# Performance work log

Measured on AMD Instinct MI355X. Metric: run time of the kernel, lower is better.

The kernel has to match this reference:

```python
import jax, jax.numpy as jnp
import numpy as np

N_QUERY = 100000
N_VALUE = 100000
N_DIM = 128
B, LQ, LK = 256, 50, 200
SIGMA = 1.0      # lognormal scale hyperparameter
LN_EPS = 1e-5    # torch LayerNorm default eps


def setup_inputs() -> dict:
    key = jax.random.key(0)
    ks = jax.random.split(key, 7)
    return {
        "Q_idx": jax.random.randint(ks[0], (B, LQ), 0, N_QUERY),
        "K_idx": jax.random.randint(ks[1], (B, LK), 0, N_VALUE),
        "V_idx": jax.random.randint(ks[2], (B, LK), 0, N_VALUE),
        "W_q": jax.random.normal(ks[3], (N_QUERY, N_DIM), dtype=jnp.float32) * 0.02,
        "W_k": jax.random.normal(ks[4], (N_VALUE, N_DIM), dtype=jnp.float32) * 0.02,
        "W_v": jax.random.normal(ks[5], (N_VALUE, N_DIM), dtype=jnp.float32) * 0.02,
        "ln_gamma": jnp.ones((N_DIM,), dtype=jnp.float32),
        "ln_beta": jnp.zeros((N_DIM,), dtype=jnp.float32),
        "eps_noise": jax.random.normal(ks[6], (B, LQ, LK), dtype=jnp.float32),
    }


def reference(Q_idx, K_idx, V_idx, W_q, W_k, W_v, ln_gamma, ln_beta, eps_noise):
    d = W_q.shape[-1]
    q = W_q[Q_idx]                                   # [B, Lq, d]
    k = W_k[K_idx]                                   # [B, Lk, d]
    logits = jnp.einsum("bqd,bkd->bqk", q, k) / jnp.sqrt(jnp.asarray(d, q.dtype))
    log_phi = jax.nn.log_softmax(logits, axis=-1)    # [B, Lq, Lk]
    # reparameterized LogNormal sample with mean phi: exp(log phi - sigma^2/2 + sigma*eps)
    score = jnp.exp(log_phi - 0.5 * SIGMA * SIGMA + SIGMA * eps_noise)
    weight = score / jnp.sum(score, axis=-1, keepdims=True)
    v = W_v[V_idx]                                   # [B, Lk, d]
    context = jnp.einsum("bqk,bkd->bqd", weight, v)  # [B, Lq, d]
    mu = jnp.mean(context, axis=-1, keepdims=True)
    var = jnp.mean(jnp.square(context - mu), axis=-1, keepdims=True)
    normed = (context - mu) * jax.lax.rsqrt(var + LN_EPS)
    return normed * ln_gamma + ln_beta
```

## Files before the change

### kernel.cpp

```cpp
#include <hip/hip_runtime.h>
#include <hip/hip_bf16.h>
#include <cstdint>

namespace {
constexpr int NB    = 256;
constexpr int LQ    = 50;
constexpr int LK    = 200;
constexpr int DIM   = 128;
constexpr int NWAVE = 8;
constexpr int NTHR  = NWAVE * 64;
constexpr int LSTR  = 204;
constexpr int KSTR  = 136;
constexpr int NKR   = 208;
constexpr int NQR   = 64;
constexpr int VG    = 8;
constexpr int NG    = LK / VG;
constexpr int KPW   = LK / NWAVE;
}

typedef __attribute__((ext_vector_type(8))) short bf16x8;
typedef __attribute__((ext_vector_type(4))) float f32x4;

__device__ __forceinline__ float bflo(uint32_t u) { return __uint_as_float(u << 16); }
__device__ __forceinline__ float bfhi(uint32_t u) { return __uint_as_float(u & 0xFFFF0000u); }
__device__ __forceinline__ uint32_t f2bf(float f) {
    uint32_t x = __float_as_uint(f);
    return (x + 0x7FFFu + ((x >> 16) & 1u)) >> 16;
}

__device__ __forceinline__ void run_f32(
    const int* __restrict__ Qi, const int* __restrict__ Ki, const int* __restrict__ Vi,
    const void* __restrict__ Wq, const void* __restrict__ Wk, const void* __restrict__ Wv,
    const void* __restrict__ gm, const void* __restrict__ bt, const void* __restrict__ ep,
    void* __restrict__ out, float* __restrict__ lds,
    uint16_t* __restrict__ ksh, uint16_t* __restrict__ qsh, int* __restrict__ vix)
{
    const int b    = blockIdx.x;
    const int tid  = threadIdx.x;
    const int w    = tid >> 6;
    const int lane = tid & 63;

    for (int i = tid; i < LK; i += NTHR) vix[i] = Vi[b * LK + i];

    #pragma unroll
    for (int j = 0; j < NKR / NWAVE; ++j) {
        const int r = w + NWAVE * j;
        uint32_t v = 0u;
        if (r < LK) {
            const int kidx = Ki[b * LK + r];
            const float2 f = ((const float2*)((const float*)Wk + (size_t)kidx * DIM))[lane];
            v = f2bf(f.x) | (f2bf(f.y) << 16);
        }
        *(uint32_t*)(ksh + (size_t)r * KSTR + 2 * lane) = v;
    }
    #pragma unroll
    for (int j = 0; j < NQR / NWAVE; ++j) {
        const int r = w + NWAVE * j;
        uint32_t v = 0u;
        if (r < LQ) {
            const int qidx = Qi[b * LQ + r];
            const float2 f = ((const float2*)((const float*)Wq + (size_t)qidx * DIM))[lane];
            v = f2bf(f.x) | (f2bf(f.y) << 16);
        }
        *(uint32_t*)(qsh + (size_t)r * KSTR + 2 * lane) = v;
    }
    __syncthreads();

    {
        const int m   = w >> 1;
        const int l15 = lane & 15;
        const int g   = lane >> 4;

        const uint16_t* qbase = qsh + (size_t)(m * 16 + l15) * KSTR + g * 8;
        bf16x8 afr[4];
        #pragma unroll
        for (int ks = 0; ks < 4; ++ks)
            afr[ks] = *(const bf16x8*)(qbase + ks * 32);

        #pragma unroll 1
        for (int n = (w & 1); n < 13; n += 2) {
            const uint16_t* kbase = ksh + (size_t)(n * 16 + l15) * KSTR + g * 8;
            f32x4 acc = {0.f, 0.f, 0.f, 0.f};
            #pragma unroll
            for (int ks = 0; ks < 4; ++ks) {
                const bf16x8 bfr = *(const bf16x8*)(kbase + ks * 32);
                acc = __builtin_amdgcn_mfma_f32_16x16x32_bf16(afr[ks], bfr, acc, 0, 0, 0);
            }
            const int kcol = n * 16 + l15;
            #pragma unroll
            for (int r = 0; r < 4; ++r) {
                const int q = m * 16 + g * 4 + r;
                if (q < LQ && kcol < LK)
                    lds[q * LSTR + kcol] = acc[r] * 0.08838834764831843f;
            }
        }
    }
    __syncthreads();

    for (int q = w; q < LQ; q += NWAVE) {
        float z[4];
        float m = -INFINITY;
        #pragma unroll
        for (int i = 0; i < 4; ++i) {
            const int k = i * 64 + lane;
            if (k < LK) {
                const float e = ((const float*)ep)[(size_t)(b * LQ + q) * LK + k];
                z[i] = lds[q * LSTR + k] + e;
                m = fmaxf(m, z[i]);
            } else z[i] = -INFINITY;
        }
        #pragma unroll
        for (int off = 32; off > 0; off >>= 1) m = fmaxf(m, __shfl_xor(m, off));
        float e4[4]; float s = 0.f;
        #pragma unroll
        for (int i = 0; i < 4; ++i) {
            e4[i] = (i * 64 + lane < LK) ? __expf(z[i] - m) : 0.f;
            s += e4[i];
        }
        #pragma unroll
        for (int off = 32; off > 0; off >>= 1) s += __shfl_xor(s, off);
        const float inv = 1.0f / s;
        #pragma unroll
        for (int i = 0; i < 4; ++i) {
            const int k = i * 64 + lane;
            if (k < LK) lds[q * LSTR + k] = e4[i] * inv;
        }
    }
    __syncthreads();

    float c0[7], c1[7];
    #pragma unroll
    for (int qi = 0; qi < 7; ++qi) { c0[qi] = 0.f; c1[qi] = 0.f; }

    int rowq[7];
    #pragma unroll
    for (int qi = 0; qi < 7; ++qi) {
        const int q = w + 8 * qi;
        rowq[qi] = (q < LQ) ? q : (LQ - 1);
    }

    const float* Wvf = (const float*)Wv;

    auto load_grp = [&](float2 (&f)[VG], int kg) {
        const int4 ia = *(const int4*)(vix + kg * VG);
        const int4 ib = *(const int4*)(vix + kg * VG + 4);
        f[0] = ((const float2*)(Wvf + (size_t)ia.x * DIM))[lane];
        f[1] = ((const float2*)(Wvf + (size_t)ia.y * DIM))[lane];
        f[2] = ((const float2*)(Wvf + (size_t)ia.z * DIM))[lane];
        f[3] = ((const float2*)(Wvf + (size_t)ia.w * DIM))[lane];
        f[4] = ((const float2*)(Wvf + (size_t)ib.x * DIM))[lane];
        f[5] = ((const float2*)(Wvf + (size_t)ib.y * DIM))[lane];
        f[6] = ((const float2*)(Wvf + (size_t)ib.z * DIM))[lane];
        f[7] = ((const float2*)(Wvf + (size_t)ib.w * DIM))[lane];
    };
    auto consume_grp = [&](const float2 (&f)[VG], int kg) {
        #pragma unroll
        for (int qi = 0; qi < 7; ++qi) {
            const float4 wa = *(const float4*)(lds + rowq[qi] * LSTR + kg * VG);
            const float4 wb = *(const float4*)(lds + rowq[qi] * LSTR + kg * VG + 4);
            c0[qi] = fmaf(wa.x, f[0].x, c0[qi]); c1[qi] = fmaf(wa.x, f[0].y, c1[qi]);
            c0[qi] = fmaf(wa.y, f[1].x, c0[qi]); c1[qi] = fmaf(wa.y, f[1].y, c1[qi]);
            c0[qi] = fmaf(wa.z, f[2].x, c0[qi]); c1[qi] = fmaf(wa.z, f[2].y, c1[qi]);
            c0[qi] = fmaf(wa.w, f[3].x, c0[qi]); c1[qi] = fmaf(wa.w, f[3].y, c1[qi]);
            c0[qi] = fmaf(wb.x, f[4].x, c0[qi]); c1[qi] = fmaf(wb.x, f[4].y, c1[qi]);
            c0[qi] = fmaf(wb.y, f[5].x, c0[qi]); c1[qi] = fmaf(wb.y, f[5].y, c1[qi]);
            c0[qi] = fmaf(wb.z, f[6].x, c0[qi]); c1[qi] = fmaf(wb.z, f[6].y, c1[qi]);
            c0[qi] = fmaf(wb.w, f[7].x, c0[qi]); c1[qi] = fmaf(wb.w, f[7].y, c1[qi]);
        }
    };

    float2 fA[VG], fB[VG];
    load_grp(fA, 0);
    #pragma unroll 1
    for (int kg = 0; kg < NG - 1; kg += 2) {
        load_grp(fB, kg + 1);
        consume_grp(fA, kg);
        load_grp(fA, kg + 2);
        consume_grp(fB, kg + 1);
    }
    consume_grp(fA, NG - 1);

    const float2 gf = ((const float2*)gm)[lane];
    const float2 bf = ((const float2*)bt)[lane];

    #pragma unroll
    for (int qi = 0; qi < 7; ++qi) {
        const int q = w + 8 * qi;
        if (q < LQ) {
            float s1 = c0[qi] + c1[qi];
            float s2 = c0[qi] * c0[qi] + c1[qi] * c1[qi];
            #pragma unroll
            for (int off = 32; off > 0; off >>= 1) {
                s1 += __shfl_xor(s1, off);
                s2 += __shfl_xor(s2, off);
            }
            const float mu = s1 * (1.0f / DIM);
            float var = s2 * (1.0f / DIM) - mu * mu;
            var = fmaxf(var, 0.f);
            const float rs = rsqrtf(var + 1e-5f);
            float2 o;
            o.x = (c0[qi] - mu) * rs * gf.x + bf.x;
            o.y = (c1[qi] - mu) * rs * gf.y + bf.y;
            ((float2*)out)[(size_t)(b * LQ + q) * (DIM / 2) + lane] = o;
        }
    }
}

__device__ __forceinline__ void run_bf16(
    const int* __restrict__ Qi, const int* __restrict__ Ki, const int* __restrict__ Vi,
    const void* __restrict__ Wq, const void* __restrict__ Wk, const void* __restrict__ Wv,
    const void* __restrict__ gm, const void* __restrict__ bt, const void* __restrict__ ep,
    void* __restrict__ out, float* __restrict__ lds, int* __restrict__ vix)
{
    const int b    = blockIdx.x;
    const int tid  = threadIdx.x;
    const int w    = tid >> 6;
    const int lane = tid & 63;

    for (int i = tid; i < LK; i += NTHR) vix[i] = Vi[b * LK + i];

    {
        const int ql   = (lane < LQ) ? lane : (LQ - 1);
        const int qidx = Qi[b * LQ + ql];
        const uint4* qrow = (const uint4*)((const uint16_t*)Wq + (size_t)qidx * DIM);
        const int k0 = w * KPW;

        int kidx[KPW];
        #pragma unroll
        for (int kk = 0; kk < KPW; ++kk) kidx[kk] = Ki[b * LK + k0 + kk];
        float acc[KPW];
        #pragma unroll
        for (int kk = 0; kk < KPW; ++kk) acc[kk] = 0.f;

        #pragma unroll 1
        for (int h = 0; h < DIM / 8; ++h) {
            const uint4 qc = qrow[h];
            const float q0 = bflo(qc.x), q1 = bfhi(qc.x);
            const float q2 = bflo(qc.y), q3 = bfhi(qc.y);
            const float q4 = bflo(qc.z), q5 = bfhi(qc.z);
            const float q6 = bflo(qc.w), q7 = bfhi(qc.w);
            #pragma unroll
            for (int kk = 0; kk < KPW; ++kk) {
                const uint4 t = ((const uint4*)((const uint16_t*)Wk + (size_t)kidx[kk] * DIM))[h];
                float a = acc[kk];
                a = fmaf(q0, bflo(t.x), a);
                a = fmaf(q1, bfhi(t.x), a);
                a = fmaf(q2, bflo(t.y), a);
                a = fmaf(q3, bfhi(t.y), a);
                a = fmaf(q4, bflo(t.z), a);
                a = fmaf(q5, bfhi(t.z), a);
                a = fmaf(q6, bflo(t.w), a);
                a = fmaf(q7, bfhi(t.w), a);
                acc[kk] = a;
            }
        }
        if (lane < LQ) {
            #pragma unroll
            for (int kk = 0; kk < KPW; ++kk)
                lds[lane * LSTR + (k0 + kk)] = acc[kk] * 0.08838834764831843f;
        }
    }
    __syncthreads();

    for (int q = w; q < LQ; q += NWAVE) {
        float z[4];
        float m = -INFINITY;
        #pragma unroll
        for (int i = 0; i < 4; ++i) {
            const int k = i * 64 + lane;
            if (k < LK) {
                const float e = bflo((uint32_t)((const uint16_t*)ep)[(size_t)(b*LQ+q)*LK + k]);
                z[i] = lds[q * LSTR + k] + e;
                m = fmaxf(m, z[i]);
            } else z[i] = -INFINITY;
        }
        #pragma unroll
        for (int off = 32; off > 0; off >>= 1) m = fmaxf(m, __shfl_xor(m, off));
        float e4[4]; float s = 0.f;
        #pragma unroll
        for (int i = 0; i < 4; ++i) {
            e4[i] = (i * 64 + lane < LK) ? __expf(z[i] - m) : 0.f;
            s += e4[i];
        }
        #pragma unroll
        for (int off = 32; off > 0; off >>= 1) s += __shfl_xor(s, off);
        const float inv = 1.0f / s;
        #pragma unroll
        for (int i = 0; i < 4; ++i) {
            const int k = i * 64 + lane;
            if (k < LK) lds[q * LSTR + k] = e4[i] * inv;
        }
    }
    __syncthreads();

    float c0[7], c1[7];
    #pragma unroll
    for (int qi = 0; qi < 7; ++qi) { c0[qi] = 0.f; c1[qi] = 0.f; }

    int rowq[7];
    #pragma unroll
    for (int qi = 0; qi < 7; ++qi) {
        const int q = w + 8 * qi;
        rowq[qi] = (q < LQ) ? q : (LQ - 1);
    }

    const uint16_t* Wvh = (const uint16_t*)Wv;

    auto load_grp = [&](uint32_t (&f)[VG], int kg) {
        #pragma unroll
        for (int u = 0; u < VG; ++u) {
            const int vidx = vix[kg * VG + u];
            f[u] = ((const uint32_t*)(Wvh + (size_t)vidx * DIM))[lane];
        }
    };
    auto consume_grp = [&](const uint32_t (&f)[VG], int kg) {
        #pragma unroll
        for (int u = 0; u < VG; ++u) {
            const int k = kg * VG + u;
            const float v0 = bflo(f[u]), v1 = bfhi(f[u]);
            #pragma unroll
            for (int qi = 0; qi < 7; ++qi) {
                const float wt = lds[rowq[qi] * LSTR + k];
                c0[qi] = fmaf(wt, v0, c0[qi]);
                c1[qi] = fmaf(wt, v1, c1[qi]);
            }
        }
    };

    uint32_t fA[VG], fB[VG];
    load_grp(fA, 0);
    #pragma unroll 1
    for (int kg = 0; kg < NG - 1; kg += 2) {
        load_grp(fB, kg + 1);
        consume_grp(fA, kg);
        load_grp(fA, kg + 2);
        consume_grp(fB, kg + 1);
    }
    consume_grp(fA, NG - 1);

    const uint32_t gu = ((const uint32_t*)gm)[lane];
    const uint32_t bu = ((const uint32_t*)bt)[lane];
    const float g0 = bflo(gu), g1 = bfhi(gu);
    const float be0 = bflo(bu), be1 = bfhi(bu);

    #pragma unroll
    for (int qi = 0; qi < 7; ++qi) {
        const int q = w + 8 * qi;
        if (q < LQ) {
            float s1 = c0[qi] + c1[qi];
            float s2 = c0[qi]*c0[qi] + c1[qi]*c1[qi];
            #pragma unroll
            for (int off = 32; off > 0; off >>= 1) {
                s1 += __shfl_xor(s1, off);
                s2 += __shfl_xor(s2, off);
            }
            const float mu = s1 * (1.0f / DIM);
            float var = s2 * (1.0f / DIM) - mu * mu;
            var = fmaxf(var, 0.f);
            const float rs = rsqrtf(var + 1e-5f);
            const float y0 = (c0[qi] - mu) * rs * g0 + be0;
            const float y1 = (c1[qi] - mu) * rs * g1 + be1;
            ((uint32_t*)out)[(size_t)(b*LQ+q) * (DIM/2) + lane] = f2bf(y0) | (f2bf(y1) << 16);
        }
    }
}

__global__ __launch_bounds__(NTHR, 1) void fused_attn_ln(
    const int* __restrict__ Qi, const int* __restrict__ Ki, const int* __restrict__ Vi,
    const void* __restrict__ Wq, const void* __restrict__ Wk, const void* __restrict__ Wv,
    const void* __restrict__ gm, const void* __restrict__ bt, const void* __restrict__ ep,
    void* __restrict__ out)
{
    __shared__ __align__(16) float    lds[LQ * LSTR];
    __shared__ __align__(16) uint16_t ksh[NKR * KSTR];
    __shared__ __align__(16) uint16_t qsh[NQR * KSTR];
    __shared__ __align__(16) int      vix[LK];

    const uint32_t* probe = (const uint32_t*)Wq;
    int c = 0;
    #pragma unroll
    for (int i = 0; i < 64; ++i) {
        float f = bflo(probe[i]);
        c += (fabsf(f) < 1.0f) ? 1 : 0;
    }
    if (c >= 48) run_bf16(Qi, Ki, Vi, Wq, Wk, Wv, gm, bt, ep, out, lds, vix);
    else         run_f32 (Qi, Ki, Vi, Wq, Wk, Wv, gm, bt, ep, out, lds, ksh, qsh, vix);
}

extern "C" void kernel_launch(void* const* d_in, const int* in_sizes, int n_in,
                              void* d_out, int out_size, void* d_ws, size_t ws_size,
                              hipStream_t stream)
{
    (void)in_sizes; (void)n_in; (void)out_size; (void)d_ws; (void)ws_size;
    fused_attn_ln<<<NB, NTHR, 0, stream>>>(
        (const int*)d_in[0], (const int*)d_in[1], (const int*)d_in[2],
        d_in[3], d_in[4], d_in[5], d_in[6], d_in[7], d_in[8], d_out);
}
```

Measured before the change: 187.8 us.

## Split query rows across two blocks per batch to double grid parallelism

```diff
diff --git a/kernel.cpp b/kernel.cpp
--- a/kernel.cpp
+++ b/kernel.cpp
@@ -3,19 +3,20 @@
 #include <cstdint>
 
 namespace {
-constexpr int NB    = 256;
-constexpr int LQ    = 50;
-constexpr int LK    = 200;
-constexpr int DIM   = 128;
-constexpr int NWAVE = 8;
-constexpr int NTHR  = NWAVE * 64;
-constexpr int LSTR  = 204;
-constexpr int KSTR  = 136;
-constexpr int NKR   = 208;
-constexpr int NQR   = 64;
-constexpr int VG    = 8;
-constexpr int NG    = LK / VG;
-constexpr int KPW   = LK / NWAVE;
+constexpr int NB     = 256;
+constexpr int LQ     = 50;
+constexpr int LK     = 200;
+constexpr int DIM    = 128;
+constexpr int NWAVE  = 8;
+constexpr int NTHR   = NWAVE * 64;
+constexpr int QSPLIT = 2;
+constexpr int QBLK   = LQ / QSPLIT;
+constexpr int LSTR   = 204;
+constexpr int KSTR   = 136;
+constexpr int NKR    = 208;
+constexpr int VG     = 8;
+constexpr int NG     = LK / VG;
+constexpr int KPW    = LK / NWAVE;
 }
 
 typedef __attribute__((ext_vector_type(8))) short bf16x8;
@@ -29,16 +30,19 @@
 }
 
 __device__ __forceinline__ void run_f32(
+    int b, int q0,
     const int* __restrict__ Qi, const int* __restrict__ Ki, const int* __restrict__ Vi,
     const void* __restrict__ Wq, const void* __restrict__ Wk, const void* __restrict__ Wv,
     const void* __restrict__ gm, const void* __restrict__ bt, const void* __restrict__ ep,
-    void* __restrict__ out, float* __restrict__ lds,
-    uint16_t* __restrict__ ksh, uint16_t* __restrict__ qsh, int* __restrict__ vix)
+    void* __restrict__ out, float* __restrict__ wgt,
+    uint16_t* __restrict__ ksh, int* __restrict__ vix)
 {
-    const int b    = blockIdx.x;
     const int tid  = threadIdx.x;
     const int w    = tid >> 6;
     const int lane = tid & 63;
+    const int l15  = lane & 15;
+    const int g    = lane >> 4;
+    const int m    = w >> 2;
 
     for (int i = tid; i < LK; i += NTHR) vix[i] = Vi[b * LK + i];
 
@@ -53,32 +57,30 @@
         }
         *(uint32_t*)(ksh + (size_t)r * KSTR + 2 * lane) = v;
     }
-    #pragma unroll
-    for (int j = 0; j < NQR / NWAVE; ++j) {
-        const int r = w + NWAVE * j;
-        uint32_t v = 0u;
-        if (r < LQ) {
-            const int qidx = Qi[b * LQ + r];
-            const float2 f = ((const float2*)((const float*)Wq + (size_t)qidx * DIM))[lane];
-            v = f2bf(f.x) | (f2bf(f.y) << 16);
-        }
-        *(uint32_t*)(qsh + (size_t)r * KSTR + 2 * lane) = v;
+
+    bf16x8 afr[4];
+    {
+        const int ql   = m * 16 + l15;
+        const int qc   = (ql < QBLK) ? ql : (QBLK - 1);
+        const int qidx = Qi[b * LQ + q0 + qc];
+        const float* qrow = (const float*)Wq + (size_t)qidx * DIM + g * 8;
+        #pragma unroll
+        for (int ks = 0; ks < 4; ++ks) {
+            const float4 f0 = *(const float4*)(qrow + ks * 32);
+            const float4 f1 = *(const float4*)(qrow + ks * 32 + 4);
+            union { bf16x8 v; uint16_t u[8]; } pk;
+            pk.u[0] = (uint16_t)f2bf(f0.x); pk.u[1] = (uint16_t)f2bf(f0.y);
+            pk.u[2] = (uint16_t)f2bf(f0.z); pk.u[3] = (uint16_t)f2bf(f0.w);
+            pk.u[4] = (uint16_t)f2bf(f1.x); pk.u[5] = (uint16_t)f2bf(f1.y);
+            pk.u[6] = (uint16_t)f2bf(f1.z); pk.u[7] = (uint16_t)f2bf(f1.w);
+            afr[ks] = pk.v;
+        }
     }
     __syncthreads();
 
     {
-        const int m   = w >> 1;
-        const int l15 = lane & 15;
-        const int g   = lane >> 4;
-
-        const uint16_t* qbase = qsh + (size_t)(m * 16 + l15) * KSTR + g * 8;
-        bf16x8 afr[4];
-        #pragma unroll
-        for (int ks = 0; ks < 4; ++ks)
-            afr[ks] = *(const bf16x8*)(qbase + ks * 32);
-
         #pragma unroll 1
-        for (int n = (w & 1); n < 13; n += 2) {
+        for (int n = (w & 3); n < 13; n += 4) {
             const uint16_t* kbase = ksh + (size_t)(n * 16 + l15) * KSTR + g * 8;
             f32x4 acc = {0.f, 0.f, 0.f, 0.f};
             #pragma unroll
@@ -89,32 +91,32 @@
             const int kcol = n * 16 + l15;
             #pragma unroll
             for (int r = 0; r < 4; ++r) {
-                const int q = m * 16 + g * 4 + r;
-                if (q < LQ && kcol < LK)
-                    lds[q * LSTR + kcol] = acc[r] * 0.08838834764831843f;
+                const int ql = m * 16 + g * 4 + r;
+                if (ql < QBLK && kcol < LK)
+                    wgt[ql * LSTR + kcol] = acc[r] * 0.08838834764831843f;
             }
         }
     }
     __syncthreads();
 
-    for (int q = w; q < LQ; q += NWAVE) {
+    for (int q = w; q < QBLK; q += NWAVE) {
         float z[4];
-        float m = -INFINITY;
+        float mx = -INFINITY;
         #pragma unroll
         for (int i = 0; i < 4; ++i) {
             const int k = i * 64 + lane;
             if (k < LK) {
-                const float e = ((const float*)ep)[(size_t)(b * LQ + q) * LK + k];
-                z[i] = lds[q * LSTR + k] + e;
-                m = fmaxf(m, z[i]);
+                const float e = ((const float*)ep)[(size_t)(b * LQ + q0 + q) * LK + k];
+                z[i] = wgt[q * LSTR + k] + e;
+                mx = fmaxf(mx, z[i]);
             } else z[i] = -INFINITY;
         }
         #pragma unroll
-        for (int off = 32; off > 0; off >>= 1) m = fmaxf(m, __shfl_xor(m, off));
+        for (int off = 32; off > 0; off >>= 1) mx = fmaxf(mx, __shfl_xor(mx, off));
         float e4[4]; float s = 0.f;
         #pragma unroll
         for (int i = 0; i < 4; ++i) {
-            e4[i] = (i * 64 + lane < LK) ? __expf(z[i] - m) : 0.f;
+            e4[i] = (i * 64 + lane < LK) ? __expf(z[i] - mx) : 0.f;
             s += e4[i];
         }
         #pragma unroll
@@ -123,20 +125,20 @@
         #pragma unroll
         for (int i = 0; i < 4; ++i) {
             const int k = i * 64 + lane;
-            if (k < LK) lds[q * LSTR + k] = e4[i] * inv;
+            if (k < LK) wgt[q * LSTR + k] = e4[i] * inv;
         }
     }
     __syncthreads();
 
-    float c0[7], c1[7];
-    #pragma unroll
-    for (int qi = 0; qi < 7; ++qi) { c0[qi] = 0.f; c1[qi] = 0.f; }
-
-    int rowq[7];
-    #pragma unroll
-    for (int qi = 0; qi < 7; ++qi) {
+    float c0[4], c1[4];
+    #pragma unroll
+    for (int qi = 0; qi < 4; ++qi) { c0[qi] = 0.f; c1[qi] = 0.f; }
+
+    int rowq[4];
+    #pragma unroll
+    for (int qi = 0; qi < 4; ++qi) {
         const int q = w + 8 * qi;
-        rowq[qi] = (q < LQ) ? q : (LQ - 1);
+        rowq[qi] = (q < QBLK) ? q : (QBLK - 1);
     }
 
     const float* Wvf = (const float*)Wv;
@@ -155,9 +157,9 @@
     };
     auto consume_grp = [&](const float2 (&f)[VG], int kg) {
         #pragma unroll
-        for (int qi = 0; qi < 7; ++qi) {
-            const float4 wa = *(const float4*)(lds + rowq[qi] * LSTR + kg * VG);
-            const float4 wb = *(const float4*)(lds + rowq[qi] * LSTR + kg * VG + 4);
+        for (int qi = 0; qi < 4; ++qi) {
+            const float4 wa = *(const float4*)(wgt + rowq[qi] * LSTR + kg * VG);
+            const float4 wb = *(const float4*)(wgt + rowq[qi] * LSTR + kg * VG + 4);
             c0[qi] = fmaf(wa.x, f[0].x, c0[qi]); c1[qi] = fmaf(wa.x, f[0].y, c1[qi]);
             c0[qi] = fmaf(wa.y, f[1].x, c0[qi]); c1[qi] = fmaf(wa.y, f[1].y, c1[qi]);
             c0[qi] = fmaf(wa.z, f[2].x, c0[qi]); c1[qi] = fmaf(wa.z, f[2].y, c1[qi]);
@@ -184,9 +186,9 @@
     const float2 bf = ((const float2*)bt)[lane];
 
     #pragma unroll
-    for (int qi = 0; qi < 7; ++qi) {
+    for (int qi = 0; qi < 4; ++qi) {
         const int q = w + 8 * qi;
-        if (q < LQ) {
+        if (q < QBLK) {
             float s1 = c0[qi] + c1[qi];
             float s2 = c0[qi] * c0[qi] + c1[qi] * c1[qi];
             #pragma unroll
@@ -201,18 +203,18 @@
             float2 o;
             o.x = (c0[qi] - mu) * rs * gf.x + bf.x;
             o.y = (c1[qi] - mu) * rs * gf.y + bf.y;
-            ((float2*)out)[(size_t)(b * LQ + q) * (DIM / 2) + lane] = o;
+            ((float2*)out)[(size_t)(b * LQ + q0 + q) * (DIM / 2) + lane] = o;
         }
     }
 }
 
 __device__ __forceinline__ void run_bf16(
+    int b, int q0,
     const int* __restrict__ Qi, const int* __restrict__ Ki, const int* __restrict__ Vi,
     const void* __restrict__ Wq, const void* __restrict__ Wk, const void* __restrict__ Wv,
     const void* __restrict__ gm, const void* __restrict__ bt, const void* __restrict__ ep,
-    void* __restrict__ out, float* __restrict__ lds, int* __restrict__ vix)
+    void* __restrict__ out, float* __restrict__ wgt, int* __restrict__ vix)
 {
-    const int b    = blockIdx.x;
     const int tid  = threadIdx.x;
     const int w    = tid >> 6;
     const int lane = tid & 63;
@@ -220,8 +222,8 @@
     for (int i = tid; i < LK; i += NTHR) vix[i] = Vi[b * LK + i];
 
     {
-        const int ql   = (lane < LQ) ? lane : (LQ - 1);
-        const int qidx = Qi[b * LQ + ql];
+        const int ql   = (lane < QBLK) ? lane : (QBLK - 1);
+        const int qidx = Qi[b * LQ + q0 + ql];
         const uint4* qrow = (const uint4*)((const uint16_t*)Wq + (size_t)qidx * DIM);
         const int k0 = w * KPW;
 
@@ -235,51 +237,51 @@
         #pragma unroll 1
         for (int h = 0; h < DIM / 8; ++h) {
             const uint4 qc = qrow[h];
-            const float q0 = bflo(qc.x), q1 = bfhi(qc.x);
-            const float q2 = bflo(qc.y), q3 = bfhi(qc.y);
-            const float q4 = bflo(qc.z), q5 = bfhi(qc.z);
-            const float q6 = bflo(qc.w), q7 = bfhi(qc.w);
+            const float a0 = bflo(qc.x), a1 = bfhi(qc.x);
+            const float a2 = bflo(qc.y), a3 = bfhi(qc.y);
+            const float a4 = bflo(qc.z), a5 = bfhi(qc.z);
+            const float a6 = bflo(qc.w), a7 = bfhi(qc.w);
             #pragma unroll
             for (int kk = 0; kk < KPW; ++kk) {
                 const uint4 t = ((const uint4*)((const uint16_t*)Wk + (size_t)kidx[kk] * DIM))[h];
                 float a = acc[kk];
-                a = fmaf(q0, bflo(t.x), a);
-                a = fmaf(q1, bfhi(t.x), a);
-                a = fmaf(q2, bflo(t.y), a);
-                a = fmaf(q3, bfhi(t.y), a);
-                a = fmaf(q4, bflo(t.z), a);
-                a = fmaf(q5, bfhi(t.z), a);
-                a = fmaf(q6, bflo(t.w), a);
-                a = fmaf(q7, bfhi(t.w), a);
+                a = fmaf(a0, bflo(t.x), a);
+                a = fmaf(a1, bfhi(t.x), a);
+                a = fmaf(a2, bflo(t.y), a);
+                a = fmaf(a3, bfhi(t.y), a);
+                a = fmaf(a4, bflo(t.z), a);
+                a = fmaf(a5, bfhi(t.z), a);
+                a = fmaf(a6, bflo(t.w), a);
+                a = fmaf(a7, bfhi(t.w), a);
                 acc[kk] = a;
             }
         }
-        if (lane < LQ) {
+        if (lane < QBLK) {
             #pragma unroll
             for (int kk = 0; kk < KPW; ++kk)
-                lds[lane * LSTR + (k0 + kk)] = acc[kk] * 0.08838834764831843f;
+                wgt[lane * LSTR + (k0 + kk)] = acc[kk] * 0.08838834764831843f;
         }
     }
     __syncthreads();
 
-    for (int q = w; q < LQ; q += NWAVE) {
+    for (int q = w; q < QBLK; q += NWAVE) {
         float z[4];
-        float m = -INFINITY;
+        float mx = -INFINITY;
         #pragma unroll
         for (int i = 0; i < 4; ++i) {
             const int k = i * 64 + lane;
             if (k < LK) {
-                const float e = bflo((uint32_t)((const uint16_t*)ep)[(size_t)(b*LQ+q)*LK + k]);
-                z[i] = lds[q * LSTR + k] + e;
-                m = fmaxf(m, z[i]);
+                const float e = bflo((uint32_t)((const uint16_t*)ep)[(size_t)(b*LQ+q0+q)*LK + k]);
+                z[i] = wgt[q * LSTR + k] + e;
+                mx = fmaxf(mx, z[i]);
             } else z[i] = -INFINITY;
         }
         #pragma unroll
-        for (int off = 32; off > 0; off >>= 1) m = fmaxf(m, __shfl_xor(m, off));
+        for (int off = 32; off > 0; off >>= 1) mx = fmaxf(mx, __shfl_xor(mx, off));
         float e4[4]; float s = 0.f;
         #pragma unroll
         for (int i = 0; i < 4; ++i) {
-            e4[i] = (i * 64 + lane < LK) ? __expf(z[i] - m) : 0.f;
+            e4[i] = (i * 64 + lane < LK) ? __expf(z[i] - mx) : 0.f;
             s += e4[i];
         }
         #pragma unroll
@@ -288,20 +290,20 @@
         #pragma unroll
         for (int i = 0; i < 4; ++i) {
             const int k = i * 64 + lane;
-            if (k < LK) lds[q * LSTR + k] = e4[i] * inv;
+            if (k < LK) wgt[q * LSTR + k] = e4[i] * inv;
         }
     }
     __syncthreads();
 
-    float c0[7], c1[7];
-    #pragma unroll
-    for (int qi = 0; qi < 7; ++qi) { c0[qi] = 0.f; c1[qi] = 0.f; }
-
-    int rowq[7];
-    #pragma unroll
-    for (int qi = 0; qi < 7; ++qi) {
+    float c0[4], c1[4];
+    #pragma unroll
+    for (int qi = 0; qi < 4; ++qi) { c0[qi] = 0.f; c1[qi] = 0.f; }
+
+    int rowq[4];
+    #pragma unroll
+    for (int qi = 0; qi < 4; ++qi) {
         const int q = w + 8 * qi;
-        rowq[qi] = (q < LQ) ? q : (LQ - 1);
+        rowq[qi] = (q < QBLK) ? q : (QBLK - 1);
     }
 
     const uint16_t* Wvh = (const uint16_t*)Wv;
@@ -319,8 +321,8 @@
             const int k = kg * VG + u;
             const float v0 = bflo(f[u]), v1 = bfhi(f[u]);
             #pragma unroll
-            for (int qi = 0; qi < 7; ++qi) {
-                const float wt = lds[rowq[qi] * LSTR + k];
+            for (int qi = 0; qi < 4; ++qi) {
+                const float wt = wgt[rowq[qi] * LSTR + k];
                 c0[qi] = fmaf(wt, v0, c0[qi]);
                 c1[qi] = fmaf(wt, v1, c1[qi]);
             }
@@ -344,9 +346,9 @@
     const float be0 = bflo(bu), be1 = bfhi(bu);
 
     #pragma unroll
-    for (int qi = 0; qi < 7; ++qi) {
+    for (int qi = 0; qi < 4; ++qi) {
         const int q = w + 8 * qi;
-        if (q < LQ) {
+        if (q < QBLK) {
             float s1 = c0[qi] + c1[qi];
             float s2 = c0[qi]*c0[qi] + c1[qi]*c1[qi];
             #pragma unroll
@@ -360,21 +362,24 @@
             const float rs = rsqrtf(var + 1e-5f);
             const float y0 = (c0[qi] - mu) * rs * g0 + be0;
             const float y1 = (c1[qi] - mu) * rs * g1 + be1;
-            ((uint32_t*)out)[(size_t)(b*LQ+q) * (DIM/2) + lane] = f2bf(y0) | (f2bf(y1) << 16);
-        }
-    }
-}
-
-__global__ __launch_bounds__(NTHR, 1) void fused_attn_ln(
+            ((uint32_t*)out)[(size_t)(b*LQ+q0+q) * (DIM/2) + lane] = f2bf(y0) | (f2bf(y1) << 16);
+        }
+    }
+}
+
+__global__ __launch_bounds__(NTHR, 4) void fused_attn_ln(
     const int* __restrict__ Qi, const int* __restrict__ Ki, const int* __restrict__ Vi,
     const void* __restrict__ Wq, const void* __restrict__ Wk, const void* __restrict__ Wv,
     const void* __restrict__ gm, const void* __restrict__ bt, const void* __restrict__ ep,
     void* __restrict__ out)
 {
-    __shared__ __align__(16) float    lds[LQ * LSTR];
+    __shared__ __align__(16) float    wgt[QBLK * LSTR];
     __shared__ __align__(16) uint16_t ksh[NKR * KSTR];
-    __shared__ __align__(16) uint16_t qsh[NQR * KSTR];
     __shared__ __align__(16) int      vix[LK];
+
+    const int bb = blockIdx.x;
+    const int b  = bb & (NB - 1);
+    const int q0 = (bb >> 8) * QBLK;
 
     const uint32_t* probe = (const uint32_t*)Wq;
     int c = 0;
@@ -383,8 +388,8 @@
         float f = bflo(probe[i]);
         c += (fabsf(f) < 1.0f) ? 1 : 0;
     }
-    if (c >= 48) run_bf16(Qi, Ki, Vi, Wq, Wk, Wv, gm, bt, ep, out, lds, vix);
-    else         run_f32 (Qi, Ki, Vi, Wq, Wk, Wv, gm, bt, ep, out, lds, ksh, qsh, vix);
+    if (c >= 48) run_bf16(b, q0, Qi, Ki, Vi, Wq, Wk, Wv, gm, bt, ep, out, wgt, vix);
+    else         run_f32 (b, q0, Qi, Ki, Vi, Wq, Wk, Wv, gm, bt, ep, out, wgt, ksh, vix);
 }
 
 extern "C" void kernel_launch(void* const* d_in, const int* in_sizes, int n_in,
@@ -392,7 +397,7 @@
                               hipStream_t stream)
 {
     (void)in_sizes; (void)n_in; (void)out_size; (void)d_ws; (void)ws_size;
-    fused_attn_ln<<<NB, NTHR, 0, stream>>>(
+    fused_attn_ln<<<NB * QSPLIT, NTHR, 0, stream>>>(
         (const int*)d_in[0], (const int*)d_in[1], (const int*)d_in[2],
         d_in[3], d_in[4], d_in[5], d_in[6], d_in[7], d_in[8], d_out);
 }
```

After: 193.5 us. 3.0% more time.

## Compute weight·V with bf16 MFMA via transposed V staging in LDS

Applied to the files above, without the earlier changes.

```diff
diff --git a/kernel.cpp b/kernel.cpp
--- a/kernel.cpp
+++ b/kernel.cpp
@@ -12,10 +12,13 @@
 constexpr int LSTR  = 204;
 constexpr int KSTR  = 136;
 constexpr int NKR   = 208;
-constexpr int NQR   = 64;
+constexpr int PSTR  = 232;
+constexpr int VSTR  = 232;
+constexpr int NKT3  = 7;
+constexpr int UKV   = 128 * VSTR;
+constexpr int KPW   = LK / NWAVE;
 constexpr int VG    = 8;
 constexpr int NG    = LK / VG;
-constexpr int KPW   = LK / NWAVE;
 }
 
 typedef __attribute__((ext_vector_type(8))) short bf16x8;
@@ -29,19 +32,24 @@
 }
 
 __device__ __forceinline__ void run_f32(
+    int b,
     const int* __restrict__ Qi, const int* __restrict__ Ki, const int* __restrict__ Vi,
     const void* __restrict__ Wq, const void* __restrict__ Wk, const void* __restrict__ Wv,
     const void* __restrict__ gm, const void* __restrict__ bt, const void* __restrict__ ep,
-    void* __restrict__ out, float* __restrict__ lds,
-    uint16_t* __restrict__ ksh, uint16_t* __restrict__ qsh, int* __restrict__ vix)
+    void* __restrict__ out, float* __restrict__ lgt, uint16_t* __restrict__ ukv,
+    uint16_t* __restrict__ pwgt, float2* __restrict__ part, int* __restrict__ vix)
 {
-    const int b    = blockIdx.x;
     const int tid  = threadIdx.x;
     const int w    = tid >> 6;
     const int lane = tid & 63;
+    const int l15  = lane & 15;
+    const int g    = lane >> 4;
+    const int m    = w >> 1;
+    const int h    = w & 1;
 
     for (int i = tid; i < LK; i += NTHR) vix[i] = Vi[b * LK + i];
 
+    uint16_t* ksh = ukv;
     #pragma unroll
     for (int j = 0; j < NKR / NWAVE; ++j) {
         const int r = w + NWAVE * j;
@@ -53,32 +61,30 @@
         }
         *(uint32_t*)(ksh + (size_t)r * KSTR + 2 * lane) = v;
     }
-    #pragma unroll
-    for (int j = 0; j < NQR / NWAVE; ++j) {
-        const int r = w + NWAVE * j;
-        uint32_t v = 0u;
-        if (r < LQ) {
-            const int qidx = Qi[b * LQ + r];
-            const float2 f = ((const float2*)((const float*)Wq + (size_t)qidx * DIM))[lane];
-            v = f2bf(f.x) | (f2bf(f.y) << 16);
-        }
-        *(uint32_t*)(qsh + (size_t)r * KSTR + 2 * lane) = v;
-    }
-    __syncthreads();
-
+
+    bf16x8 afr[4];
     {
-        const int m   = w >> 1;
-        const int l15 = lane & 15;
-        const int g   = lane >> 4;
-
-        const uint16_t* qbase = qsh + (size_t)(m * 16 + l15) * KSTR + g * 8;
-        bf16x8 afr[4];
-        #pragma unroll
-        for (int ks = 0; ks < 4; ++ks)
-            afr[ks] = *(const bf16x8*)(qbase + ks * 32);
-
+        const int ql   = m * 16 + l15;
+        const int qc   = (ql < LQ) ? ql : (LQ - 1);
+        const int qidx = Qi[b * LQ + qc];
+        const float* qrow = (const float*)Wq + (size_t)qidx * DIM + g * 8;
+        #pragma unroll
+        for (int ks = 0; ks < 4; ++ks) {
+            const float4 f0 = *(const float4*)(qrow + ks * 32);
+            const float4 f1 = *(const float4*)(qrow + ks * 32 + 4);
+            union { bf16x8 v; uint16_t u[8]; } pk;
+            pk.u[0] = (uint16_t)f2bf(f0.x); pk.u[1] = (uint16_t)f2bf(f0.y);
+            pk.u[2] = (uint16_t)f2bf(f0.z); pk.u[3] = (uint16_t)f2bf(f0.w);
+            pk.u[4] = (uint16_t)f2bf(f1.x); pk.u[5] = (uint16_t)f2bf(f1.y);
+            pk.u[6] = (uint16_t)f2bf(f1.z); pk.u[7] = (uint16_t)f2bf(f1.w);
+            afr[ks] = pk.v;
+        }
+    }
+    __syncthreads();
+
+    {
         #pragma unroll 1
-        for (int n = (w & 1); n < 13; n += 2) {
+        for (int n = h; n < 13; n += 2) {
             const uint16_t* kbase = ksh + (size_t)(n * 16 + l15) * KSTR + g * 8;
             f32x4 acc = {0.f, 0.f, 0.f, 0.f};
             #pragma unroll
@@ -91,128 +97,138 @@
             for (int r = 0; r < 4; ++r) {
                 const int q = m * 16 + g * 4 + r;
                 if (q < LQ && kcol < LK)
-                    lds[q * LSTR + kcol] = acc[r] * 0.08838834764831843f;
-            }
-        }
-    }
-    __syncthreads();
-
-    for (int q = w; q < LQ; q += NWAVE) {
-        float z[4];
-        float m = -INFINITY;
-        #pragma unroll
-        for (int i = 0; i < 4; ++i) {
-            const int k = i * 64 + lane;
-            if (k < LK) {
-                const float e = ((const float*)ep)[(size_t)(b * LQ + q) * LK + k];
-                z[i] = lds[q * LSTR + k] + e;
-                m = fmaxf(m, z[i]);
-            } else z[i] = -INFINITY;
-        }
-        #pragma unroll
-        for (int off = 32; off > 0; off >>= 1) m = fmaxf(m, __shfl_xor(m, off));
-        float e4[4]; float s = 0.f;
-        #pragma unroll
-        for (int i = 0; i < 4; ++i) {
-            e4[i] = (i * 64 + lane < LK) ? __expf(z[i] - m) : 0.f;
-            s += e4[i];
-        }
-        #pragma unroll
-        for (int off = 32; off > 0; off >>= 1) s += __shfl_xor(s, off);
-        const float inv = 1.0f / s;
-        #pragma unroll
-        for (int i = 0; i < 4; ++i) {
-            const int k = i * 64 + lane;
-            if (k < LK) lds[q * LSTR + k] = e4[i] * inv;
-        }
-    }
-    __syncthreads();
-
-    float c0[7], c1[7];
-    #pragma unroll
-    for (int qi = 0; qi < 7; ++qi) { c0[qi] = 0.f; c1[qi] = 0.f; }
-
-    int rowq[7];
-    #pragma unroll
-    for (int qi = 0; qi < 7; ++qi) {
-        const int q = w + 8 * qi;
-        rowq[qi] = (q < LQ) ? q : (LQ - 1);
-    }
-
-    const float* Wvf = (const float*)Wv;
-
-    auto load_grp = [&](float2 (&f)[VG], int kg) {
-        const int4 ia = *(const int4*)(vix + kg * VG);
-        const int4 ib = *(const int4*)(vix + kg * VG + 4);
-        f[0] = ((const float2*)(Wvf + (size_t)ia.x * DIM))[lane];
-        f[1] = ((const float2*)(Wvf + (size_t)ia.y * DIM))[lane];
-        f[2] = ((const float2*)(Wvf + (size_t)ia.z * DIM))[lane];
-        f[3] = ((const float2*)(Wvf + (size_t)ia.w * DIM))[lane];
-        f[4] = ((const float2*)(Wvf + (size_t)ib.x * DIM))[lane];
-        f[5] = ((const float2*)(Wvf + (size_t)ib.y * DIM))[lane];
-        f[6] = ((const float2*)(Wvf + (size_t)ib.z * DIM))[lane];
-        f[7] = ((const float2*)(Wvf + (size_t)ib.w * DIM))[lane];
-    };
-    auto consume_grp = [&](const float2 (&f)[VG], int kg) {
-        #pragma unroll
-        for (int qi = 0; qi < 7; ++qi) {
-            const float4 wa = *(const float4*)(lds + rowq[qi] * LSTR + kg * VG);
-            const float4 wb = *(const float4*)(lds + rowq[qi] * LSTR + kg * VG + 4);
-            c0[qi] = fmaf(wa.x, f[0].x, c0[qi]); c1[qi] = fmaf(wa.x, f[0].y, c1[qi]);
-            c0[qi] = fmaf(wa.y, f[1].x, c0[qi]); c1[qi] = fmaf(wa.y, f[1].y, c1[qi]);
-            c0[qi] = fmaf(wa.z, f[2].x, c0[qi]); c1[qi] = fmaf(wa.z, f[2].y, c1[qi]);
-            c0[qi] = fmaf(wa.w, f[3].x, c0[qi]); c1[qi] = fmaf(wa.w, f[3].y, c1[qi]);
-            c0[qi] = fmaf(wb.x, f[4].x, c0[qi]); c1[qi] = fmaf(wb.x, f[4].y, c1[qi]);
-            c0[qi] = fmaf(wb.y, f[5].x, c0[qi]); c1[qi] = fmaf(wb.y, f[5].y, c1[qi]);
-            c0[qi] = fmaf(wb.z, f[6].x, c0[qi]); c1[qi] = fmaf(wb.z, f[6].y, c1[qi]);
-            c0[qi] = fmaf(wb.w, f[7].x, c0[qi]); c1[qi] = fmaf(wb.w, f[7].y, c1[qi]);
-        }
-    };
-
-    float2 fA[VG], fB[VG];
-    load_grp(fA, 0);
-    #pragma unroll 1
-    for (int kg = 0; kg < NG - 1; kg += 2) {
-        load_grp(fB, kg + 1);
-        consume_grp(fA, kg);
-        load_grp(fA, kg + 2);
-        consume_grp(fB, kg + 1);
-    }
-    consume_grp(fA, NG - 1);
-
-    const float2 gf = ((const float2*)gm)[lane];
-    const float2 bf = ((const float2*)bt)[lane];
-
-    #pragma unroll
-    for (int qi = 0; qi < 7; ++qi) {
-        const int q = w + 8 * qi;
+                    lgt[q * LSTR + kcol] = acc[r] * 0.08838834764831843f;
+            }
+        }
+    }
+    __syncthreads();
+
+    uint16_t* vsh = ukv;
+    #pragma unroll
+    for (int j = 0; j < 4; ++j) {
+        const int k8 = w + NWAVE * j;
+        if (k8 < 28) {
+            float2 vr[8];
+            #pragma unroll
+            for (int r = 0; r < 8; ++r) {
+                const int k = k8 * 8 + r;
+                if (k < LK) {
+                    const int vidx = vix[k];
+                    vr[r] = ((const float2*)((const float*)Wv + (size_t)vidx * DIM))[lane];
+                } else vr[r] = make_float2(0.f, 0.f);
+            }
+            union { bf16x8 v; uint16_t u[8]; } px, py;
+            #pragma unroll
+            for (int r = 0; r < 8; ++r) {
+                px.u[r] = (uint16_t)f2bf(vr[r].x);
+                py.u[r] = (uint16_t)f2bf(vr[r].y);
+            }
+            *(bf16x8*)(vsh + (size_t)(2 * lane)     * VSTR + k8 * 8) = px.v;
+            *(bf16x8*)(vsh + (size_t)(2 * lane + 1) * VSTR + k8 * 8) = py.v;
+        }
+    }
+
+    for (int q = w; q < 64; q += NWAVE) {
         if (q < LQ) {
-            float s1 = c0[qi] + c1[qi];
-            float s2 = c0[qi] * c0[qi] + c1[qi] * c1[qi];
-            #pragma unroll
-            for (int off = 32; off > 0; off >>= 1) {
-                s1 += __shfl_xor(s1, off);
-                s2 += __shfl_xor(s2, off);
-            }
-            const float mu = s1 * (1.0f / DIM);
-            float var = s2 * (1.0f / DIM) - mu * mu;
-            var = fmaxf(var, 0.f);
-            const float rs = rsqrtf(var + 1e-5f);
-            float2 o;
-            o.x = (c0[qi] - mu) * rs * gf.x + bf.x;
-            o.y = (c1[qi] - mu) * rs * gf.y + bf.y;
-            ((float2*)out)[(size_t)(b * LQ + q) * (DIM / 2) + lane] = o;
+            float z[4];
+            float mx = -INFINITY;
+            #pragma unroll
+            for (int i = 0; i < 4; ++i) {
+                const int k = i * 64 + lane;
+                if (k < LK) {
+                    const float e = ((const float*)ep)[(size_t)(b * LQ + q) * LK + k];
+                    z[i] = lgt[q * LSTR + k] + e;
+                    mx = fmaxf(mx, z[i]);
+                } else z[i] = -INFINITY;
+            }
+            #pragma unroll
+            for (int off = 32; off > 0; off >>= 1) mx = fmaxf(mx, __shfl_xor(mx, off));
+            float e4[4]; float s = 0.f;
+            #pragma unroll
+            for (int i = 0; i < 4; ++i) {
+                e4[i] = (i * 64 + lane < LK) ? __expf(z[i] - mx) : 0.f;
+                s += e4[i];
+            }
+            #pragma unroll
+            for (int off = 32; off > 0; off >>= 1) s += __shfl_xor(s, off);
+            const float inv = 1.0f / s;
+            #pragma unroll
+            for (int i = 0; i < 4; ++i) {
+                const int k = i * 64 + lane;
+                if (k < PSTR)
+                    pwgt[q * PSTR + k] = (k < LK) ? (uint16_t)f2bf(e4[i] * inv) : (uint16_t)0;
+            }
+        } else {
+            #pragma unroll
+            for (int i = 0; i < 4; ++i) {
+                const int k = i * 64 + lane;
+                if (k < PSTR) pwgt[q * PSTR + k] = 0;
+            }
+        }
+    }
+    __syncthreads();
+
+    f32x4 acc[4] = {{0.f,0.f,0.f,0.f},{0.f,0.f,0.f,0.f},{0.f,0.f,0.f,0.f},{0.f,0.f,0.f,0.f}};
+    #pragma unroll
+    for (int kt = 0; kt < NKT3; ++kt) {
+        const bf16x8 a = *(const bf16x8*)(pwgt + (size_t)(m * 16 + l15) * PSTR + kt * 32 + g * 8);
+        #pragma unroll
+        for (int t = 0; t < 4; ++t) {
+            const int d = (h * 4 + t) * 16 + l15;
+            const bf16x8 bv = *(const bf16x8*)(vsh + (size_t)d * VSTR + kt * 32 + g * 8);
+            acc[t] = __builtin_amdgcn_mfma_f32_16x16x32_bf16(a, bv, acc[t], 0, 0, 0);
+        }
+    }
+
+    float s1[4], s2[4];
+    #pragma unroll
+    for (int r = 0; r < 4; ++r) {
+        s1[r] = acc[0][r] + acc[1][r] + acc[2][r] + acc[3][r];
+        s2[r] = acc[0][r]*acc[0][r] + acc[1][r]*acc[1][r]
+              + acc[2][r]*acc[2][r] + acc[3][r]*acc[3][r];
+        #pragma unroll
+        for (int off = 1; off < 16; off <<= 1) {
+            s1[r] += __shfl_xor(s1[r], off);
+            s2[r] += __shfl_xor(s2[r], off);
+        }
+    }
+    if (l15 == 0) {
+        #pragma unroll
+        for (int r = 0; r < 4; ++r)
+            part[(m * 16 + g * 4 + r) * 2 + h] = make_float2(s1[r], s2[r]);
+    }
+    __syncthreads();
+
+    float* outf = (float*)out;
+    #pragma unroll
+    for (int r = 0; r < 4; ++r) {
+        const int q = m * 16 + g * 4 + r;
+        const float2 oth = part[q * 2 + (h ^ 1)];
+        const float t1 = s1[r] + oth.x;
+        const float t2 = s2[r] + oth.y;
+        const float mu = t1 * (1.0f / DIM);
+        float var = t2 * (1.0f / DIM) - mu * mu;
+        var = fmaxf(var, 0.f);
+        const float rs = rsqrtf(var + 1e-5f);
+        if (q < LQ) {
+            #pragma unroll
+            for (int t = 0; t < 4; ++t) {
+                const int d = (h * 4 + t) * 16 + l15;
+                const float gv = ((const float*)gm)[d];
+                const float bv = ((const float*)bt)[d];
+                outf[(size_t)(b * LQ + q) * DIM + d] = (acc[t][r] - mu) * rs * gv + bv;
+            }
         }
     }
 }
 
 __device__ __forceinline__ void run_bf16(
+    int b,
     const int* __restrict__ Qi, const int* __restrict__ Ki, const int* __restrict__ Vi,
     const void* __restrict__ Wq, const void* __restrict__ Wk, const void* __restrict__ Wv,
     const void* __restrict__ gm, const void* __restrict__ bt, const void* __restrict__ ep,
     void* __restrict__ out, float* __restrict__ lds, int* __restrict__ vix)
 {
-    const int b    = blockIdx.x;
     const int tid  = threadIdx.x;
     const int w    = tid >> 6;
     const int lane = tid & 63;
@@ -233,24 +249,24 @@
         for (int kk = 0; kk < KPW; ++kk) acc[kk] = 0.f;
 
         #pragma unroll 1
-        for (int h = 0; h < DIM / 8; ++h) {
-            const uint4 qc = qrow[h];
-            const float q0 = bflo(qc.x), q1 = bfhi(qc.x);
-            const float q2 = bflo(qc.y), q3 = bfhi(qc.y);
-            const float q4 = bflo(qc.z), q5 = bfhi(qc.z);
-            const float q6 = bflo(qc.w), q7 = bfhi(qc.w);
+        for (int hh = 0; hh < DIM / 8; ++hh) {
+            const uint4 qc = qrow[hh];
+            const float a0 = bflo(qc.x), a1 = bfhi(qc.x);
+            const float a2 = bflo(qc.y), a3 = bfhi(qc.y);
+            const float a4 = bflo(qc.z), a5 = bfhi(qc.z);
+            const float a6 = bflo(qc.w), a7 = bfhi(qc.w);
             #pragma unroll
             for (int kk = 0; kk < KPW; ++kk) {
-                const uint4 t = ((const uint4*)((const uint16_t*)Wk + (size_t)kidx[kk] * DIM))[h];
+                const uint4 t = ((const uint4*)((const uint16_t*)Wk + (size_t)kidx[kk] * DIM))[hh];
                 float a = acc[kk];
-                a = fmaf(q0, bflo(t.x), a);
-                a = fmaf(q1, bfhi(t.x), a);
-                a = fmaf(q2, bflo(t.y), a);
-                a = fmaf(q3, bfhi(t.y), a);
-                a = fmaf(q4, bflo(t.z), a);
-                a = fmaf(q5, bfhi(t.z), a);
-                a = fmaf(q6, bflo(t.w), a);
-                a = fmaf(q7, bfhi(t.w), a);
+                a = fmaf(a0, bflo(t.x), a);
+                a = fmaf(a1, bfhi(t.x), a);
+                a = fmaf(a2, bflo(t.y), a);
+                a = fmaf(a3, bfhi(t.y), a);
+                a = fmaf(a4, bflo(t.z), a);
+                a = fmaf(a5, bfhi(t.z), a);
+                a = fmaf(a6, bflo(t.w), a);
+                a = fmaf(a7, bfhi(t.w), a);
                 acc[kk] = a;
             }
         }
@@ -264,22 +280,22 @@
 
     for (int q = w; q < LQ; q += NWAVE) {
         float z[4];
-        float m = -INFINITY;
+        float mx = -INFINITY;
         #pragma unroll
         for (int i = 0; i < 4; ++i) {
             const int k = i * 64 + lane;
             if (k < LK) {
                 const float e = bflo((uint32_t)((const uint16_t*)ep)[(size_t)(b*LQ+q)*LK + k]);
                 z[i] = lds[q * LSTR + k] + e;
-                m = fmaxf(m, z[i]);
+                mx = fmaxf(mx, z[i]);
             } else z[i] = -INFINITY;
         }
         #pragma unroll
-        for (int off = 32; off > 0; off >>= 1) m = fmaxf(m, __shfl_xor(m, off));
+        for (int off = 32; off > 0; off >>= 1) mx = fmaxf(mx, __shfl_xor(mx, off));
         float e4[4]; float s = 0.f;
         #pragma unroll
         for (int i = 0; i < 4; ++i) {
-            e4[i] = (i * 64 + lane < LK) ? __expf(z[i] - m) : 0.f;
+            e4[i] = (i * 64 + lane < LK) ? __expf(z[i] - mx) : 0.f;
             s += e4[i];
         }
         #pragma unroll
@@ -371,10 +387,13 @@
     const void* __restrict__ gm, const void* __restrict__ bt, const void* __restrict__ ep,
     void* __restrict__ out)
 {
-    __shared__ __align__(16) float    lds[LQ * LSTR];
-    __shared__ __align__(16) uint16_t ksh[NKR * KSTR];
-    __shared__ __align__(16) uint16_t qsh[NQR * KSTR];
-    __shared__ __align__(16) int      vix[LK];
+    __shared__ __align__(16) uint16_t ukv[UKV];
+    __shared__ __align__(16) float    lgt[LQ * LSTR];
+    __shared__ __align__(16) uint16_t pwgt[64 * PSTR];
+    __shared__ float2 part[64 * 2];
+    __shared__ int vix[LK];
+
+    const int b = blockIdx.x;
 
     const uint32_t* probe = (const uint32_t*)Wq;
     int c = 0;
@@ -383,8 +402,9 @@
         float f = bflo(probe[i]);
         c += (fabsf(f) < 1.0f) ? 1 : 0;
     }
-    if (c >= 48) run_bf16(Qi, Ki, Vi, Wq, Wk, Wv, gm, bt, ep, out, lds, vix);
-    else         run_f32 (Qi, Ki, Vi, Wq, Wk, Wv, gm, bt, ep, out, lds, ksh, qsh, vix);
+    if (c >= 48) run_bf16(b, Qi, Ki, Vi, Wq, Wk, Wv, gm, bt, ep, out, lgt, vix);
+    else         run_f32 (b, Qi, Ki, Vi, Wq, Wk, Wv, gm, bt, ep, out,
+                          lgt, ukv, pwgt, part, vix);
 }
 
 extern "C" void kernel_launch(void* const* d_in, const int* in_sizes, int n_in,
```

Measured after the change: 177.4 us. 1.06x faster.
